# Kernel tuning notes

Measured on AMD Instinct MI355X. Metric: run time of the kernel, lower is better.

The kernel has to match this reference:

```python
import jax, jax.numpy as jnp
import numpy as np

B, S, D = 4, 2048, 1024
H, DH = 16, 64  # d_model = H*DH = 1024
NEG = 1e10


def setup_inputs() -> dict:
    key = jax.random.key(0)
    ks = jax.random.split(key, 5)
    scale = 1.0 / np.sqrt(D)
    x = jax.random.normal(ks[0], (B, S, D), dtype=jnp.float32)
    mask = jax.random.randint(ks[1], (B, S), 0, 2).astype(jnp.float32)
    Wq = jax.random.normal(ks[2], (D, H * DH), dtype=jnp.float32) * scale
    Wk = jax.random.normal(ks[3], (D, H * DH), dtype=jnp.float32) * scale
    Wv = jax.random.normal(ks[4], (D, H * DH), dtype=jnp.float32) * scale
    z = jnp.zeros((H * DH,), dtype=jnp.float32)
    return {"x": x, "mask": mask, "Wq": Wq, "bq": z, "Wk": Wk, "bk": z,
            "Wv": Wv, "bv": z}


def reference(x, mask, Wq, bq, Wk, bk, Wv, bv):
    # projections -> [B, H, S, DH]
    def proj(W, b):
        y = x @ W + b
        return y.reshape(B, S, H, DH).transpose(0, 2, 1, 3)

    q, k, v = proj(Wq, bq), proj(Wk, bk), proj(Wv, bv)
    scores = jnp.einsum("bhsd,bhtd->bhst", q, k) / np.sqrt(DH)
    m = mask[:, None, None, :]                      # [B,1,1,S]
    scores = scores - (1.0 - m) * NEG               # additive mask
    probs = jax.nn.softmax(scores, axis=-1)         # stable (max-subtract)
    probs = probs * m                               # multiplicative mask
    out = jnp.einsum("bhst,bhtd->bhsd", probs, v)   # [B,H,S,DH]
    return out.transpose(0, 2, 1, 3).reshape(B, S, H * DH)
```

## Files before the change

kernel.cpp:

```cpp
#include <hip/hip_runtime.h>

typedef float f32x4 __attribute__((ext_vector_type(4)));
typedef float f32x16 __attribute__((ext_vector_type(16)));
typedef _Float16 f16;
typedef _Float16 f16x2 __attribute__((ext_vector_type(2)));
typedef _Float16 f16x8 __attribute__((ext_vector_type(8)));
typedef unsigned int u32x2 __attribute__((ext_vector_type(2)));
typedef unsigned short u16;
typedef unsigned short u16x4 __attribute__((ext_vector_type(4)));
typedef unsigned int u32;

#define S_LEN 2048
#define NHEAD 16
#define DHEAD 64
#define DMODEL 1024
#define NBATCH 4

__device__ __forceinline__ void gload16(const u16* g, const uint4* l) {
  __builtin_amdgcn_global_load_lds((const __attribute__((address_space(1))) void*)g,
                                   (__attribute__((address_space(3))) void*)l, 16, 0, 0);
}


__device__ __forceinline__ float dot2acc(u32 a, u32 b, float c) {
#if __has_builtin(__builtin_amdgcn_fdot2)
  return __builtin_amdgcn_fdot2(__builtin_bit_cast(f16x2, a), __builtin_bit_cast(f16x2, b), c, false);
#else
  f16x2 pa = __builtin_bit_cast(f16x2, a), pb = __builtin_bit_cast(f16x2, b);
  return c + (float)pa[0] * (float)pb[0] + (float)pa[1] * (float)pb[1];
#endif
}

__global__ void cvt_x(const float* __restrict__ x, u16* __restrict__ o, int n4) {
  int i = blockIdx.x * blockDim.x + threadIdx.x;
  int st = gridDim.x * blockDim.x;
  for (; i < n4; i += st) {
    float4 v = reinterpret_cast<const float4*>(x)[i];
    uint2 r;
    r.x = __builtin_bit_cast(u32, __builtin_amdgcn_cvt_pkrtz(v.x, v.y));
    r.y = __builtin_bit_cast(u32, __builtin_amdgcn_cvt_pkrtz(v.z, v.w));
    reinterpret_cast<uint2*>(o)[i] = r;
  }
}

__global__ void trans_w(const float* __restrict__ W, u16* __restrict__ wt) {
  __shared__ float t[32][33];
  int bx = blockIdx.x * 32, by = blockIdx.y * 32;
  int tx = threadIdx.x & 31, ty = threadIdx.x >> 5;
#pragma unroll
  for (int i = 0; i < 32; i += 8)
    t[ty + i][tx] = W[(size_t)(by + ty + i) * DMODEL + bx + tx];
  __syncthreads();
#pragma unroll
  for (int i = 0; i < 32; i += 8)
    wt[(size_t)(bx + ty + i) * DMODEL + by + tx] = __builtin_bit_cast(u16, (f16)t[tx][ty + i]);
}

__global__ __launch_bounds__(256) void qkv_gemm(
    const u16* __restrict__ A, const u16* __restrict__ Wt,
    const float* __restrict__ bq, const float* __restrict__ bk, const float* __restrict__ bv,
    const float* __restrict__ mask,
    u16* __restrict__ Qo, u16* __restrict__ Ko, u16* __restrict__ Vo)
{
  __shared__ uint4 As4[3][512];
  __shared__ uint4 Bs4[3][512];
  const int tid = threadIdx.x;
  const int lane = tid & 63;
  const int wid = tid >> 6;
  const int l31 = lane & 31, hi = lane >> 5;
  const int m0 = blockIdx.x * 128;
  const int n0 = blockIdx.y * 128;
  const int wr = (wid >> 1) * 64, wc = (wid & 1) * 64;

  f32x16 acc[2][2] = {};

  const int c0 = wid * 64 + lane, c1 = c0 + 256;
  const int r0 = c0 >> 2, r1 = c1 >> 2;
  const int p4 = lane & 3;
  const int sl0 = p4 ^ ((r0 >> 1) & 3);
  const int sl1 = p4 ^ ((r1 >> 1) & 3);
  const u16* ag0 = A  + (size_t)(m0 + r0) * 1024 + sl0 * 8;
  const u16* ag1 = A  + (size_t)(m0 + r1) * 1024 + sl1 * 8;
  const u16* bg0 = Wt + (size_t)(n0 + r0) * 1024 + sl0 * 8;
  const u16* bg1 = Wt + (size_t)(n0 + r1) * 1024 + sl1 * 8;

  auto stage = [&](int buf, int kt) {
    gload16(ag0 + kt, &As4[buf][wid * 64]);
    gload16(ag1 + kt, &As4[buf][wid * 64 + 256]);
    gload16(bg0 + kt, &Bs4[buf][wid * 64]);
    gload16(bg1 + kt, &Bs4[buf][wid * 64 + 256]);
  };

  int aoff[2][2], boff[2][2];
#pragma unroll
  for (int mi = 0; mi < 2; mi++) {
    int r = wr + mi * 32 + l31;
#pragma unroll
    for (int ks = 0; ks < 2; ks++)
      aoff[mi][ks] = r * 32 + (((ks * 2 + hi) ^ ((r >> 1) & 3)) * 8);
  }
#pragma unroll
  for (int ni = 0; ni < 2; ni++) {
    int r = wc + ni * 32 + l31;
#pragma unroll
    for (int ks = 0; ks < 2; ks++)
      boff[ni][ks] = r * 32 + (((ks * 2 + hi) ^ ((r >> 1) & 3)) * 8);
  }

  stage(0, 0);
  stage(1, 32);
  __syncthreads();

  const int NT = 1024 / 32;
  for (int it = 0; it < NT; ++it) {
    if (it + 1 < NT) asm volatile("s_waitcnt vmcnt(4)" ::: "memory");
    else             asm volatile("s_waitcnt vmcnt(0)" ::: "memory");
    __builtin_amdgcn_s_barrier();
    __builtin_amdgcn_sched_barrier(0);
    const int cur = it % 3;
    if (it + 2 < NT) stage((it + 2) % 3, (it + 2) * 32);

    const u16* As = (const u16*)&As4[cur][0];
    const u16* Bs = (const u16*)&Bs4[cur][0];
    f16x8 af[2][2], bf[2][2];
#pragma unroll
    for (int mi = 0; mi < 2; mi++)
#pragma unroll
      for (int ks = 0; ks < 2; ks++)
        af[mi][ks] = *(const f16x8*)&As[aoff[mi][ks]];
#pragma unroll
    for (int ni = 0; ni < 2; ni++)
#pragma unroll
      for (int ks = 0; ks < 2; ks++)
        bf[ni][ks] = *(const f16x8*)&Bs[boff[ni][ks]];

#pragma unroll
    for (int ks = 0; ks < 2; ks++)
#pragma unroll
      for (int mi = 0; mi < 2; mi++)
#pragma unroll
        for (int ni = 0; ni < 2; ni++)
          acc[mi][ni] = __builtin_amdgcn_mfma_f32_32x32x16_f16(af[mi][ks], bf[ni][ks], acc[mi][ni], 0, 0, 0);
  }

  const int sel = n0 >> 10;
  const float* bias = (sel == 0) ? bq : (sel == 1) ? bk : bv;
  const int nbase = (n0 & 1023) + wc;
  const float QSCALE = 0.18033688011112042f;
#pragma unroll
  for (int mi = 0; mi < 2; mi++)
#pragma unroll
    for (int ni = 0; ni < 2; ni++) {
      const int ncol = nbase + ni * 32 + l31;
      const float bi = bias[ncol];
      const int h = ncol >> 6, dh = ncol & 63;
#pragma unroll
      for (int r4 = 0; r4 < 4; r4++) {
        const int rowb = m0 + wr + mi * 32 + 8 * r4 + 4 * hi;
        const int bb = rowb >> 11, s0 = rowb & 2047;
        const size_t bh = (size_t)(bb * NHEAD + h);
        if (sel == 0) {
#pragma unroll
          for (int j = 0; j < 4; j++)
            Qo[(bh * S_LEN + s0 + j) * DHEAD + dh] =
                __builtin_bit_cast(u16, (f16)((acc[mi][ni][r4 * 4 + j] + bi) * QSCALE));
        } else if (sel == 1) {
#pragma unroll
          for (int j = 0; j < 4; j++)
            Ko[(bh * S_LEN + s0 + j) * DHEAD + dh] =
                __builtin_bit_cast(u16, (f16)(acc[mi][ni][r4 * 4 + j] + bi));
        } else {
          const float4 mk = *(const float4*)&mask[bb * S_LEN + s0];
          u16x4 pk;
#pragma unroll
          for (int j = 0; j < 4; j++) {
            float v = acc[mi][ni][r4 * 4 + j] + bi;
            float mj = (j == 0) ? mk.x : (j == 1) ? mk.y : (j == 2) ? mk.z : mk.w;
            if (mj <= 0.f) v = 0.f;
            pk[j] = __builtin_bit_cast(u16, (f16)v);
          }
          *(u16x4*)&Vo[(bh * DHEAD + dh) * S_LEN + s0] = pk;
        }
      }
    }
}

__global__ __launch_bounds__(256, 2) void attn(
    const u16* __restrict__ Q, const u16* __restrict__ K, const u16* __restrict__ Vt,
    const float* __restrict__ mask, float* __restrict__ out)
{
  __shared__ uint4 Ks4[3][512];
  __shared__ uint4 Vs4[3][512];
  __shared__ __align__(16) u16 MsAll[S_LEN];
  const int tid = threadIdx.x;
  const int lane = tid & 63, wid = tid >> 6;
  const int l31 = lane & 31, hi = lane >> 5;
  const int sid = blockIdx.x;
  const int qt = (sid >> 3) & 7;
  const int bh = (sid & 7) + 8 * (sid >> 6);
  const int b = bh >> 4, h = bh & 15;
  const size_t base = (size_t)bh * S_LEN * DHEAD;
  const u16* Qp = Q + base;
  const u16* Kp = K + base;
  const u16* Vp = Vt + base;
  const float* mp = mask + b * S_LEN;
  const int q0 = qt * 256 + wid * 64;

  f16x8 aqA[4], aqB[4];
#pragma unroll
  for (int kc = 0; kc < 4; kc++) {
    aqA[kc] = *(const f16x8*)&Qp[(size_t)(q0 + l31) * DHEAD + kc * 16 + hi * 8];
    aqB[kc] = *(const f16x8*)&Qp[(size_t)(q0 + 32 + l31) * DHEAD + kc * 16 + hi * 8];
  }

  f32x16 accO0A = {}, accO1A = {};
  f32x16 accO0B = {}, accO1B = {};
  float lA = 0.f, lB = 0.f;

  const int cA_ = wid * 128 + lane, cB_ = cA_ + 64;
  const int rk0 = cA_ >> 3, rk1 = cB_ >> 3;
  const int p8 = lane & 7;
  const int cc0 = (p8 - ((rk0 + (rk0 >> 3)) & 7)) & 7;
  const int cc1 = (p8 - ((rk1 + (rk1 >> 3)) & 7)) & 7;
  const u16* kg0 = Kp + (size_t)rk0 * DHEAD + cc0 * 8;
  const u16* kg1 = Kp + (size_t)rk1 * DHEAD + cc1 * 8;
  const u16* vg0 = Vp + (size_t)rk0 * S_LEN + cc0 * 8;
  const u16* vg1 = Vp + (size_t)rk1 * S_LEN + cc1 * 8;

  auto stage = [&](int buf) {
    gload16(kg0, &Ks4[buf][wid * 128]); gload16(kg1, &Ks4[buf][wid * 128 + 64]);
    gload16(vg0, &Vs4[buf][wid * 128]); gload16(vg1, &Vs4[buf][wid * 128 + 64]);
    kg0 += 64 * DHEAD; kg1 += 64 * DHEAD; vg0 += 64; vg1 += 64;
  };

  const int swA = (l31 + (l31 >> 3)) & 7;
  const int swB = (swA + 4) & 7;
  int idxA[4], idxB[4];
#pragma unroll
  for (int kc = 0; kc < 4; kc++) {
    idxA[kc] = l31 * 8 + ((kc * 2 + hi + swA) & 7);
    idxB[kc] = (32 + l31) * 8 + ((kc * 2 + hi + swB) & 7);
  }

  {
    float4 ml0 = *(const float4*)&mp[tid * 8];
    float4 ml1 = *(const float4*)&mp[tid * 8 + 4];
    uint4 w;
    w.x = __builtin_bit_cast(u32, __builtin_amdgcn_cvt_pkrtz(ml0.x, ml0.y));
    w.y = __builtin_bit_cast(u32, __builtin_amdgcn_cvt_pkrtz(ml0.z, ml0.w));
    w.z = __builtin_bit_cast(u32, __builtin_amdgcn_cvt_pkrtz(ml1.x, ml1.y));
    w.w = __builtin_bit_cast(u32, __builtin_amdgcn_cvt_pkrtz(ml1.z, ml1.w));
    *(uint4*)&MsAll[tid * 8] = w;
  }
  stage(0);
  stage(1);
  __syncthreads();

  const int NT = S_LEN / 64;
  for (int it = 0; it < NT; ++it) {
    if (it + 1 < NT) asm volatile("s_waitcnt vmcnt(4)" ::: "memory");
    else             asm volatile("s_waitcnt vmcnt(0)" ::: "memory");
    __builtin_amdgcn_s_barrier();
    __builtin_amdgcn_sched_barrier(0);
    const int cur = it % 3;
    const uint4* ks = &Ks4[cur][0];
    const uint4* vs = &Vs4[cur][0];
    if (it + 2 < NT) stage((it + 2) % 3);

    f32x16 sA0 = {}, sA1 = {}, sB0 = {}, sB1 = {};
    __builtin_amdgcn_s_setprio(1);
#pragma unroll
    for (int kc = 0; kc < 4; kc++) {
      f16x8 k0 = *(const f16x8*)&ks[idxA[kc]];
      f16x8 k1 = *(const f16x8*)&ks[idxB[kc]];
      sA0 = __builtin_amdgcn_mfma_f32_32x32x16_f16(k0, aqA[kc], sA0, 0, 0, 0);
      sA1 = __builtin_amdgcn_mfma_f32_32x32x16_f16(k1, aqA[kc], sA1, 0, 0, 0);
      sB0 = __builtin_amdgcn_mfma_f32_32x32x16_f16(k0, aqB[kc], sB0, 0, 0, 0);
      sB1 = __builtin_amdgcn_mfma_f32_32x32x16_f16(k1, aqB[kc], sB1, 0, 0, 0);
    }
    __builtin_amdgcn_s_setprio(0);

#pragma unroll
    for (int g = 0; g < 4; g++) {
      const f32x16& srcA = (g < 2) ? sA0 : sA1;
      const f32x16& srcB = (g < 2) ? sB0 : sB1;
      const int o = (g & 1) * 8;
      u32 wa[4], wb[4];
#pragma unroll
      for (int s = 0; s < 4; s++) {
        wa[s] = __builtin_bit_cast(u32, __builtin_amdgcn_cvt_pkrtz(
                    __builtin_amdgcn_exp2f(srcA[o + 2 * s]),
                    __builtin_amdgcn_exp2f(srcA[o + 2 * s + 1])));
        wb[s] = __builtin_bit_cast(u32, __builtin_amdgcn_cvt_pkrtz(
                    __builtin_amdgcn_exp2f(srcB[o + 2 * s]),
                    __builtin_amdgcn_exp2f(srcB[o + 2 * s + 1])));
      }
      u32x2 rA0 = __builtin_amdgcn_permlane32_swap(wa[0], wa[2], false, false);
      u32x2 rA1 = __builtin_amdgcn_permlane32_swap(wa[1], wa[3], false, false);
      u32x2 rB0 = __builtin_amdgcn_permlane32_swap(wb[0], wb[2], false, false);
      u32x2 rB1 = __builtin_amdgcn_permlane32_swap(wb[1], wb[3], false, false);
      uint4 f4A; f4A.x = rA0[0]; f4A.y = rA1[0]; f4A.z = rA0[1]; f4A.w = rA1[1];
      uint4 f4B; f4B.x = rB0[0]; f4B.y = rB1[0]; f4B.z = rB0[1]; f4B.w = rB1[1];
      f16x8 fA = __builtin_bit_cast(f16x8, f4A);
      f16x8 fB = __builtin_bit_cast(f16x8, f4B);
      f16x8 bv0 = *(const f16x8*)&vs[idxA[g]];
      f16x8 bv1 = *(const f16x8*)&vs[idxB[g]];
      const uint4 bmw = *(const uint4*)&MsAll[it * 64 + g * 16 + hi * 8];
      __builtin_amdgcn_s_setprio(1);
      accO0A = __builtin_amdgcn_mfma_f32_32x32x16_f16(fA, bv0, accO0A, 0, 0, 0);
      accO1A = __builtin_amdgcn_mfma_f32_32x32x16_f16(fA, bv1, accO1A, 0, 0, 0);
      accO0B = __builtin_amdgcn_mfma_f32_32x32x16_f16(fB, bv0, accO0B, 0, 0, 0);
      accO1B = __builtin_amdgcn_mfma_f32_32x32x16_f16(fB, bv1, accO1B, 0, 0, 0);
      __builtin_amdgcn_s_setprio(0);
      lA = dot2acc(f4A.x, bmw.x, lA);
      lA = dot2acc(f4A.y, bmw.y, lA);
      lA = dot2acc(f4A.z, bmw.z, lA);
      lA = dot2acc(f4A.w, bmw.w, lA);
      lB = dot2acc(f4B.x, bmw.x, lB);
      lB = dot2acc(f4B.y, bmw.y, lB);
      lB = dot2acc(f4B.z, bmw.z, lB);
      lB = dot2acc(f4B.w, bmw.w, lB);
    }
  }

  float lAf = lA + __shfl_xor(lA, 32, 64);
  float lBf = lB + __shfl_xor(lB, 32, 64);
  float invA = (lAf > 0.f) ? 1.f / lAf : 0.f;
  float invB = (lBf > 0.f) ? 1.f / lBf : 0.f;
#pragma unroll
  for (int r = 0; r < 16; r++) {
    int qr = (r & 3) + 8 * (r >> 2) + 4 * hi;
    float iA = __builtin_bit_cast(float,
        (u32)__builtin_amdgcn_ds_bpermute(qr << 2, (int)__builtin_bit_cast(u32, invA)));
    float iB = __builtin_bit_cast(float,
        (u32)__builtin_amdgcn_ds_bpermute(qr << 2, (int)__builtin_bit_cast(u32, invB)));
    float* opA = out + ((size_t)(b * S_LEN + q0 + qr) * DMODEL) + h * DHEAD;
    float* opB = out + ((size_t)(b * S_LEN + q0 + 32 + qr) * DMODEL) + h * DHEAD;
    opA[l31] = accO0A[r] * iA;
    opA[32 + l31] = accO1A[r] * iA;
    opB[l31] = accO0B[r] * iB;
    opB[32 + l31] = accO1B[r] * iB;
  }
}

extern "C" void kernel_launch(void* const* d_in, const int* in_sizes, int n_in,
                              void* d_out, int out_size, void* d_ws, size_t ws_size,
                              hipStream_t stream) {
  const float* x    = (const float*)d_in[0];
  const float* mask = (const float*)d_in[1];
  const float* Wq   = (const float*)d_in[2];
  const float* bq   = (const float*)d_in[3];
  const float* Wk   = (const float*)d_in[4];
  const float* bk   = (const float*)d_in[5];
  const float* Wv   = (const float*)d_in[6];
  const float* bv   = (const float*)d_in[7];
  float* out = (float*)d_out;

  u16* xb = (u16*)d_ws;
  u16* wt = xb + (size_t)8192 * 1024;
  u16* Qb = wt + (size_t)3072 * 1024;
  u16* Kb = Qb + (size_t)8388608;
  u16* Vb = Kb + (size_t)8388608;

  cvt_x<<<2048, 256, 0, stream>>>(x, xb, (8192 * 1024) / 4);
  trans_w<<<dim3(32, 32), 256, 0, stream>>>(Wq, wt);
  trans_w<<<dim3(32, 32), 256, 0, stream>>>(Wk, wt + (size_t)1024 * 1024);
  trans_w<<<dim3(32, 32), 256, 0, stream>>>(Wv, wt + (size_t)2 * 1024 * 1024);
  qkv_gemm<<<dim3(64, 24), 256, 0, stream>>>(xb, wt, bq, bk, bv, mask, Qb, Kb, Vb);
  attn<<<512, 256, 0, stream>>>(Qb, Kb, Vb, mask, out);
}
```

Baseline: 169.0 us.

## Software-pipeline QK^T of next tile with PV of current tile

Restructures the attention main loop so the QK^T MFMAs for tile it+1 are issued alongside the exp/PV work for tile it, letting matrix and vector work interleave across iterations. The row-sum accumulator is split into four independent partial sums to shorten the dependent dot2 chain, and the setprio hints are removed. The cost is more live registers (an extra set of four score accumulators), which risks spills or lower occupancy. The wait is tightened to vmcnt(0) every iteration, so the prefetch of tile it+2 is no longer allowed to stay in flight across the barrier.

```diff
diff --git a/kernel.cpp b/kernel.cpp
--- a/kernel.cpp
+++ b/kernel.cpp
@@ -215,7 +215,8 @@
 
   f32x16 accO0A = {}, accO1A = {};
   f32x16 accO0B = {}, accO1B = {};
-  float lA = 0.f, lB = 0.f;
+  float lAp[4] = {0.f, 0.f, 0.f, 0.f};
+  float lBp[4] = {0.f, 0.f, 0.f, 0.f};
 
   const int cA_ = wid * 128 + lane, cB_ = cA_ + 64;
   const int rk0 = cA_ >> 3, rk1 = cB_ >> 3;
@@ -256,34 +257,25 @@
   stage(1);
   __syncthreads();
 
-  const int NT = S_LEN / 64;
-  for (int it = 0; it < NT; ++it) {
-    if (it + 1 < NT) asm volatile("s_waitcnt vmcnt(4)" ::: "memory");
-    else             asm volatile("s_waitcnt vmcnt(0)" ::: "memory");
-    __builtin_amdgcn_s_barrier();
-    __builtin_amdgcn_sched_barrier(0);
-    const int cur = it % 3;
-    const uint4* ks = &Ks4[cur][0];
-    const uint4* vs = &Vs4[cur][0];
-    if (it + 2 < NT) stage((it + 2) % 3);
-
-    f32x16 sA0 = {}, sA1 = {}, sB0 = {}, sB1 = {};
-    __builtin_amdgcn_s_setprio(1);
+  f32x16 pA0 = {}, pA1 = {}, pB0 = {}, pB1 = {};
+
+  auto qkt = [&](const uint4* ks, f32x16& A0, f32x16& A1, f32x16& B0, f32x16& B1) {
 #pragma unroll
     for (int kc = 0; kc < 4; kc++) {
       f16x8 k0 = *(const f16x8*)&ks[idxA[kc]];
       f16x8 k1 = *(const f16x8*)&ks[idxB[kc]];
-      sA0 = __builtin_amdgcn_mfma_f32_32x32x16_f16(k0, aqA[kc], sA0, 0, 0, 0);
-      sA1 = __builtin_amdgcn_mfma_f32_32x32x16_f16(k1, aqA[kc], sA1, 0, 0, 0);
-      sB0 = __builtin_amdgcn_mfma_f32_32x32x16_f16(k0, aqB[kc], sB0, 0, 0, 0);
-      sB1 = __builtin_amdgcn_mfma_f32_32x32x16_f16(k1, aqB[kc], sB1, 0, 0, 0);
+      A0 = __builtin_amdgcn_mfma_f32_32x32x16_f16(k0, aqA[kc], A0, 0, 0, 0);
+      A1 = __builtin_amdgcn_mfma_f32_32x32x16_f16(k1, aqA[kc], A1, 0, 0, 0);
+      B0 = __builtin_amdgcn_mfma_f32_32x32x16_f16(k0, aqB[kc], B0, 0, 0, 0);
+      B1 = __builtin_amdgcn_mfma_f32_32x32x16_f16(k1, aqB[kc], B1, 0, 0, 0);
     }
-    __builtin_amdgcn_s_setprio(0);
-
+  };
+
+  auto phaseB = [&](const uint4* vs, int it) {
 #pragma unroll
     for (int g = 0; g < 4; g++) {
-      const f32x16& srcA = (g < 2) ? sA0 : sA1;
-      const f32x16& srcB = (g < 2) ? sB0 : sB1;
+      const f32x16& srcA = (g < 2) ? pA0 : pA1;
+      const f32x16& srcB = (g < 2) ? pB0 : pB1;
       const int o = (g & 1) * 8;
       u32 wa[4], wb[4];
 #pragma unroll
@@ -306,23 +298,39 @@
       f16x8 bv0 = *(const f16x8*)&vs[idxA[g]];
       f16x8 bv1 = *(const f16x8*)&vs[idxB[g]];
       const uint4 bmw = *(const uint4*)&MsAll[it * 64 + g * 16 + hi * 8];
-      __builtin_amdgcn_s_setprio(1);
       accO0A = __builtin_amdgcn_mfma_f32_32x32x16_f16(fA, bv0, accO0A, 0, 0, 0);
       accO1A = __builtin_amdgcn_mfma_f32_32x32x16_f16(fA, bv1, accO1A, 0, 0, 0);
       accO0B = __builtin_amdgcn_mfma_f32_32x32x16_f16(fB, bv0, accO0B, 0, 0, 0);
       accO1B = __builtin_amdgcn_mfma_f32_32x32x16_f16(fB, bv1, accO1B, 0, 0, 0);
-      __builtin_amdgcn_s_setprio(0);
-      lA = dot2acc(f4A.x, bmw.x, lA);
-      lA = dot2acc(f4A.y, bmw.y, lA);
-      lA = dot2acc(f4A.z, bmw.z, lA);
-      lA = dot2acc(f4A.w, bmw.w, lA);
-      lB = dot2acc(f4B.x, bmw.x, lB);
-      lB = dot2acc(f4B.y, bmw.y, lB);
-      lB = dot2acc(f4B.z, bmw.z, lB);
-      lB = dot2acc(f4B.w, bmw.w, lB);
+      lAp[0] = dot2acc(f4A.x, bmw.x, lAp[0]);
+      lAp[1] = dot2acc(f4A.y, bmw.y, lAp[1]);
+      lAp[2] = dot2acc(f4A.z, bmw.z, lAp[2]);
+      lAp[3] = dot2acc(f4A.w, bmw.w, lAp[3]);
+      lBp[0] = dot2acc(f4B.x, bmw.x, lBp[0]);
+      lBp[1] = dot2acc(f4B.y, bmw.y, lBp[1]);
+      lBp[2] = dot2acc(f4B.z, bmw.z, lBp[2]);
+      lBp[3] = dot2acc(f4B.w, bmw.w, lBp[3]);
     }
-  }
-
+  };
+
+  qkt(&Ks4[0][0], pA0, pA1, pB0, pB1);
+
+  const int NT = S_LEN / 64;
+  for (int it = 0; it < NT - 1; ++it) {
+    asm volatile("s_waitcnt vmcnt(0)" ::: "memory");
+    __builtin_amdgcn_s_barrier();
+    __builtin_amdgcn_sched_barrier(0);
+    const int cur = it % 3, nxt = (it + 1) % 3;
+    if (it + 2 < NT) stage((it + 2) % 3);
+    f32x16 nA0 = {}, nA1 = {}, nB0 = {}, nB1 = {};
+    qkt(&Ks4[nxt][0], nA0, nA1, nB0, nB1);
+    phaseB(&Vs4[cur][0], it);
+    pA0 = nA0; pA1 = nA1; pB0 = nB0; pB1 = nB1;
+  }
+  phaseB(&Vs4[(NT - 1) % 3][0], NT - 1);
+
+  float lA = (lAp[0] + lAp[1]) + (lAp[2] + lAp[3]);
+  float lB = (lBp[0] + lBp[1]) + (lBp[2] + lBp[3]);
   float lAf = lA + __shfl_xor(lA, 32, 64);
   float lBf = lB + __shfl_xor(lB, 32, 64);
   float invA = (lAf > 0.f) ? 1.f / lAf : 0.f;
```

Measured after the change: 168.1 us. About the same (-0.6%).
